# Optimization experiments

Hardware: AMD Instinct MI355X
Metric: run time of the kernel (lower is better)

The kernel has to match this reference:

```python
import jax, jax.numpy as jnp
import numpy as np

BATCH, IN_WIDTH, OUT_FEATURES, FAN_IN = 512, 4096, 4096, 128

def setup_inputs() -> dict:
    key = jax.random.key(0)
    k1, k2, k3, k4 = jax.random.split(key, 4)
    input = jax.random.normal(k1, (BATCH, IN_WIDTH), dtype=jnp.float32)
    weight = jax.random.normal(k2, (OUT_FEATURES, FAN_IN), dtype=jnp.float32)
    bias = jax.random.normal(k3, (OUT_FEATURES,), dtype=jnp.float32)
    indx_seqs = jax.random.randint(k4, (OUT_FEATURES, FAN_IN), 0, IN_WIDTH, dtype=jnp.int64)
    return {"input": input, "weight": weight, "bias": bias, "indx_seqs": indx_seqs}

def reference(input, weight, bias, indx_seqs):
    # gather: (B, out_features, fan_in)
    gathered = input[:, indx_seqs]
    # elementwise mul with weight (out_features, fan_in), reduce over fan_in
    return jnp.einsum('bof,of->bo', gathered, weight) + bias
```

## Files before the change

### kernel.cpp

```cpp
#include <hip/hip_runtime.h>
#include <hip/hip_bf16.h>

#define BATCH    512
#define IN_WIDTH 4096
#define OUT_F    4096
#define FAN_IN   128
#define BCHUNK   16
#define NBG      (BATCH / BCHUNK)
#define OBLK     512
#define NOG      (OUT_F / OBLK)

__global__ __launch_bounds__(256) void k_transpose_in(const float* __restrict__ in,
                                                      uint16_t* __restrict__ inTg) {
  __shared__ float tile[32][33];
  const int jt = blockIdx.x * 32;
  const int bt = blockIdx.y * 32;
  const int tx = threadIdx.x;
  const int ty = threadIdx.y;
#pragma unroll
  for (int r = 0; r < 32; r += 8) {
    tile[ty + r][tx] = in[(size_t)(bt + ty + r) * IN_WIDTH + (jt + tx)];
  }
  __syncthreads();
#pragma unroll
  for (int r = 0; r < 32; r += 8) {
    const int b = bt + tx;
    const int j = jt + ty + r;
    __hip_bfloat16 hv = __float2bfloat16(tile[tx][ty + r]);
    inTg[((size_t)(b >> 4) * IN_WIDTH + j) * BCHUNK + (b & 15)] =
        *reinterpret_cast<const uint16_t*>(&hv);
  }
}

__global__ __launch_bounds__(256) void k_pack(const int* __restrict__ idx,
                                              const float* __restrict__ weight,
                                              uint2* __restrict__ pk) {
  const int i = blockIdx.x * 256 + threadIdx.x;
  uint2 e;
  e.x = (uint32_t)idx[i];
  e.y = __float_as_uint(weight[i]);
  pk[i] = e;
}

__global__ __launch_bounds__(1024, 1) void k_gather_lds(const uint16_t* __restrict__ inTg,
                                                        const uint2* __restrict__ pk,
                                                        const float* __restrict__ bias,
                                                        float* __restrict__ outT) {
  extern __shared__ uint16_t inS[];
  const int og = blockIdx.x;
  const int bg = blockIdx.y;
  const int t  = threadIdx.x;

  {
    const uint4* __restrict__ src =
        reinterpret_cast<const uint4*>(inTg + (size_t)bg * IN_WIDTH * BCHUNK);
    uint4* dst = reinterpret_cast<uint4*>(inS);
#pragma unroll
    for (int i = 0; i < 8; ++i) {
      dst[i * 1024 + t] = src[i * 1024 + t];
    }
  }
  __syncthreads();

  const int wv = t >> 6;
  const int l  = t & 63;
  const int o  = og * OBLK + wv * 32 + (l >> 1);
  const int p  = l & 1;

  const uint4* __restrict__ pko = reinterpret_cast<const uint4*>(pk + (size_t)o * FAN_IN);
  const char* rowbase = reinterpret_cast<const char*>(inS) + p * 16;

  float a0 = 0.f, a1 = 0.f, a2 = 0.f, a3 = 0.f;
  float a4 = 0.f, a5 = 0.f, a6 = 0.f, a7 = 0.f;

#pragma unroll 2
  for (int f2 = 0; f2 < FAN_IN / 2; ++f2) {
    const uint4 q = pko[f2];
    {
      const uint4 v = *reinterpret_cast<const uint4*>(rowbase + q.x * 32);
      const float w = __uint_as_float(q.y);
      a0 = fmaf(__uint_as_float(v.x << 16),          w, a0);
      a1 = fmaf(__uint_as_float(v.x & 0xffff0000u),  w, a1);
      a2 = fmaf(__uint_as_float(v.y << 16),          w, a2);
      a3 = fmaf(__uint_as_float(v.y & 0xffff0000u),  w, a3);
      a4 = fmaf(__uint_as_float(v.z << 16),          w, a4);
      a5 = fmaf(__uint_as_float(v.z & 0xffff0000u),  w, a5);
      a6 = fmaf(__uint_as_float(v.w << 16),          w, a6);
      a7 = fmaf(__uint_as_float(v.w & 0xffff0000u),  w, a7);
    }
    {
      const uint4 v = *reinterpret_cast<const uint4*>(rowbase + q.z * 32);
      const float w = __uint_as_float(q.w);
      a0 = fmaf(__uint_as_float(v.x << 16),          w, a0);
      a1 = fmaf(__uint_as_float(v.x & 0xffff0000u),  w, a1);
      a2 = fmaf(__uint_as_float(v.y << 16),          w, a2);
      a3 = fmaf(__uint_as_float(v.y & 0xffff0000u),  w, a3);
      a4 = fmaf(__uint_as_float(v.z << 16),          w, a4);
      a5 = fmaf(__uint_as_float(v.z & 0xffff0000u),  w, a5);
      a6 = fmaf(__uint_as_float(v.w << 16),          w, a6);
      a7 = fmaf(__uint_as_float(v.w & 0xffff0000u),  w, a7);
    }
  }

  const float bz = bias[o];
  float4 r0 = make_float4(a0 + bz, a1 + bz, a2 + bz, a3 + bz);
  float4 r1 = make_float4(a4 + bz, a5 + bz, a6 + bz, a7 + bz);
  float4* dst = reinterpret_cast<float4*>(outT + (size_t)o * BATCH + bg * BCHUNK + p * 8);
  dst[0] = r0;
  dst[1] = r1;
}

__global__ __launch_bounds__(256) void k_transpose_out(const float* __restrict__ outT,
                                                       float* __restrict__ out) {
  __shared__ float tile[32][33];
  const int ot = blockIdx.x * 32;
  const int bt = blockIdx.y * 32;
  const int tx = threadIdx.x;
  const int ty = threadIdx.y;
#pragma unroll
  for (int r = 0; r < 32; r += 8) {
    tile[ty + r][tx] = outT[(size_t)(ot + ty + r) * BATCH + (bt + tx)];
  }
  __syncthreads();
#pragma unroll
  for (int r = 0; r < 32; r += 8) {
    out[(size_t)(bt + ty + r) * OUT_F + (ot + tx)] = tile[tx][ty + r];
  }
}

extern "C" void kernel_launch(void* const* d_in, const int* in_sizes, int n_in,
                              void* d_out, int out_size, void* d_ws, size_t ws_size,
                              hipStream_t stream) {
  const float* input  = (const float*)d_in[0];
  const float* weight = (const float*)d_in[1];
  const float* bias   = (const float*)d_in[2];
  const int*   idx    = (const int*)d_in[3];
  float* out = (float*)d_out;

  uint16_t* inTg = (uint16_t*)d_ws;
  float*    outT = (float*)((char*)d_ws + 4u * 1024 * 1024);
  uint2*    pk   = (uint2*)((char*)d_ws + 12u * 1024 * 1024);

  dim3 tblk(32, 8);
  k_transpose_in<<<dim3(IN_WIDTH / 32, BATCH / 32), tblk, 0, stream>>>(input, inTg);
  k_pack<<<dim3(OUT_F * FAN_IN / 256), dim3(256), 0, stream>>>(idx, weight, pk);
  k_gather_lds<<<dim3(NOG, NBG), dim3(1024), IN_WIDTH * BCHUNK * sizeof(uint16_t), stream>>>(
      inTg, pk, bias, outT);
  k_transpose_out<<<dim3(OUT_F / 32, BATCH / 32), tblk, 0, stream>>>(outT, out);
}
```

Before: 42.82 us.

## Fuse output transpose into gather kernel and pipeline LDS reads with packed FMA

Drops the separate output-transpose kernel and its intermediate buffer. The gather kernel now writes directly to the batch-major output with strided per-element stores. The inner loop is rewritten with inline ds_read_b128 and prefetching of the next index/weight chunk across an explicit waitcnt barrier. Accumulation uses 2-wide float vectors so the compiler can emit packed FMAs. This saves a launch and an output round trip through memory, but the direct stores write only one float per row per lane and are poorly coalesced.

```diff
diff --git a/kernel.cpp b/kernel.cpp
--- a/kernel.cpp
+++ b/kernel.cpp
@@ -9,6 +9,9 @@
 #define NBG      (BATCH / BCHUNK)
 #define OBLK     512
 #define NOG      (OUT_F / OBLK)
+
+typedef float    v2f __attribute__((ext_vector_type(2)));
+typedef uint32_t v4u __attribute__((ext_vector_type(4)));
 
 __global__ __launch_bounds__(256) void k_transpose_in(const float* __restrict__ in,
                                                       uint16_t* __restrict__ inTg) {
@@ -45,20 +48,18 @@
 __global__ __launch_bounds__(1024, 1) void k_gather_lds(const uint16_t* __restrict__ inTg,
                                                         const uint2* __restrict__ pk,
                                                         const float* __restrict__ bias,
-                                                        float* __restrict__ outT) {
-  extern __shared__ uint16_t inS[];
+                                                        float* __restrict__ out) {
+  extern __shared__ char lds[];
   const int og = blockIdx.x;
   const int bg = blockIdx.y;
   const int t  = threadIdx.x;
 
   {
-    const uint4* __restrict__ src =
-        reinterpret_cast<const uint4*>(inTg + (size_t)bg * IN_WIDTH * BCHUNK);
-    uint4* dst = reinterpret_cast<uint4*>(inS);
+    const v4u* __restrict__ src =
+        reinterpret_cast<const v4u*>(inTg + (size_t)bg * IN_WIDTH * BCHUNK);
+    v4u* dst = reinterpret_cast<v4u*>(lds);
 #pragma unroll
-    for (int i = 0; i < 8; ++i) {
-      dst[i * 1024 + t] = src[i * 1024 + t];
-    }
+    for (int i = 0; i < 8; ++i) dst[i * 1024 + t] = src[i * 1024 + t];
   }
   __syncthreads();
 
@@ -67,65 +68,71 @@
   const int o  = og * OBLK + wv * 32 + (l >> 1);
   const int p  = l & 1;
 
-  const uint4* __restrict__ pko = reinterpret_cast<const uint4*>(pk + (size_t)o * FAN_IN);
-  const char* rowbase = reinterpret_cast<const char*>(inS) + p * 16;
+  const uint32_t sb = (uint32_t)(size_t)lds + (uint32_t)(p * 16);
 
-  float a0 = 0.f, a1 = 0.f, a2 = 0.f, a3 = 0.f;
-  float a4 = 0.f, a5 = 0.f, a6 = 0.f, a7 = 0.f;
+  const v4u* __restrict__ pko =
+      reinterpret_cast<const v4u*>(pk + (size_t)o * FAN_IN);
 
-#pragma unroll 2
-  for (int f2 = 0; f2 < FAN_IN / 2; ++f2) {
-    const uint4 q = pko[f2];
-    {
-      const uint4 v = *reinterpret_cast<const uint4*>(rowbase + q.x * 32);
-      const float w = __uint_as_float(q.y);
-      a0 = fmaf(__uint_as_float(v.x << 16),          w, a0);
-      a1 = fmaf(__uint_as_float(v.x & 0xffff0000u),  w, a1);
-      a2 = fmaf(__uint_as_float(v.y << 16),          w, a2);
-      a3 = fmaf(__uint_as_float(v.y & 0xffff0000u),  w, a3);
-      a4 = fmaf(__uint_as_float(v.z << 16),          w, a4);
-      a5 = fmaf(__uint_as_float(v.z & 0xffff0000u),  w, a5);
-      a6 = fmaf(__uint_as_float(v.w << 16),          w, a6);
-      a7 = fmaf(__uint_as_float(v.w & 0xffff0000u),  w, a7);
-    }
-    {
-      const uint4 v = *reinterpret_cast<const uint4*>(rowbase + q.z * 32);
-      const float w = __uint_as_float(q.w);
-      a0 = fmaf(__uint_as_float(v.x << 16),          w, a0);
-      a1 = fmaf(__uint_as_float(v.x & 0xffff0000u),  w, a1);
-      a2 = fmaf(__uint_as_float(v.y << 16),          w, a2);
-      a3 = fmaf(__uint_as_float(v.y & 0xffff0000u),  w, a3);
-      a4 = fmaf(__uint_as_float(v.z << 16),          w, a4);
-      a5 = fmaf(__uint_as_float(v.z & 0xffff0000u),  w, a5);
-      a6 = fmaf(__uint_as_float(v.w << 16),          w, a6);
-      a7 = fmaf(__uint_as_float(v.w & 0xffff0000u),  w, a7);
-    }
+  v2f a0 = {0.f, 0.f}, a1 = {0.f, 0.f}, a2 = {0.f, 0.f}, a3 = {0.f, 0.f};
+
+#define DSREAD(dst, jj) \
+  asm volatile("ds_read_b128 %0, %1" : "=v"(dst) : "v"(sb + ((jj) << 5)))
+
+#define CONSUME(v, wbits)                                              \
+  do {                                                                 \
+    const float wf_ = __uint_as_float(wbits);                          \
+    v2f w2_; w2_[0] = wf_; w2_[1] = wf_;                               \
+    v2f x0_, x1_, x2_, x3_;                                            \
+    x0_[0] = __uint_as_float((v).x << 16);                             \
+    x0_[1] = __uint_as_float((v).x & 0xffff0000u);                     \
+    x1_[0] = __uint_as_float((v).y << 16);                             \
+    x1_[1] = __uint_as_float((v).y & 0xffff0000u);                     \
+    x2_[0] = __uint_as_float((v).z << 16);                             \
+    x2_[1] = __uint_as_float((v).z & 0xffff0000u);                     \
+    x3_[0] = __uint_as_float((v).w << 16);                             \
+    x3_[1] = __uint_as_float((v).w & 0xffff0000u);                     \
+    a0 += x0_ * w2_; a1 += x1_ * w2_; a2 += x2_ * w2_; a3 += x3_ * w2_;\
+  } while (0)
+
+#define HALF(qq0, qq1, qq2, qq3, nextchunk, more)                      \
+  do {                                                                 \
+    v4u v0, v1, v2, v3, v4, v5, v6, v7;                                \
+    DSREAD(v0, qq0.x); DSREAD(v1, qq0.z);                              \
+    DSREAD(v2, qq1.x); DSREAD(v3, qq1.z);                              \
+    DSREAD(v4, qq2.x); DSREAD(v5, qq2.z);                              \
+    DSREAD(v6, qq3.x); DSREAD(v7, qq3.z);                              \
+    const uint32_t w0 = qq0.y, w1 = qq0.w, w2 = qq1.y, w3 = qq1.w;     \
+    const uint32_t w4 = qq2.y, w5 = qq2.w, w6 = qq3.y, w7 = qq3.w;     \
+    if (more) {                                                        \
+      qq0 = pko[(nextchunk) * 4 + 0];                                  \
+      qq1 = pko[(nextchunk) * 4 + 1];                                  \
+      qq2 = pko[(nextchunk) * 4 + 2];                                  \
+      qq3 = pko[(nextchunk) * 4 + 3];                                  \
+    }                                                                  \
+    asm volatile("s_waitcnt lgkmcnt(0)" ::: "memory");                 \
+    __builtin_amdgcn_sched_barrier(0);                                 \
+    CONSUME(v0, w0); CONSUME(v1, w1); CONSUME(v2, w2); CONSUME(v3, w3);\
+    CONSUME(v4, w4); CONSUME(v5, w5); CONSUME(v6, w6); CONSUME(v7, w7);\
+  } while (0)
+
+  v4u qa0 = pko[0], qa1 = pko[1], qa2 = pko[2], qa3 = pko[3];
+  v4u qb0 = pko[4], qb1 = pko[5], qb2 = pko[6], qb3 = pko[7];
+
+#pragma unroll 1
+  for (int c = 0; c < 8; ++c) {
+    HALF(qa0, qa1, qa2, qa3, 2 * c + 2, (c < 7));
+    HALF(qb0, qb1, qb2, qb3, 2 * c + 3, (c < 7));
   }
 
   const float bz = bias[o];
-  float4 r0 = make_float4(a0 + bz, a1 + bz, a2 + bz, a3 + bz);
-  float4 r1 = make_float4(a4 + bz, a5 + bz, a6 + bz, a7 + bz);
-  float4* dst = reinterpret_cast<float4*>(outT + (size_t)o * BATCH + bg * BCHUNK + p * 8);
-  dst[0] = r0;
-  dst[1] = r1;
-}
+  const float r[8] = {a0[0], a0[1], a1[0], a1[1], a2[0], a2[1], a3[0], a3[1]};
+  const size_t obase = (size_t)(bg * BCHUNK + p * 8) * OUT_F + o;
+#pragma unroll
+  for (int i = 0; i < 8; ++i) out[obase + (size_t)i * OUT_F] = r[i] + bz;
 
-__global__ __launch_bounds__(256) void k_transpose_out(const float* __restrict__ outT,
-                                                       float* __restrict__ out) {
-  __shared__ float tile[32][33];
-  const int ot = blockIdx.x * 32;
-  const int bt = blockIdx.y * 32;
-  const int tx = threadIdx.x;
-  const int ty = threadIdx.y;
-#pragma unroll
-  for (int r = 0; r < 32; r += 8) {
-    tile[ty + r][tx] = outT[(size_t)(ot + ty + r) * BATCH + (bt + tx)];
-  }
-  __syncthreads();
-#pragma unroll
-  for (int r = 0; r < 32; r += 8) {
-    out[(size_t)(bt + ty + r) * OUT_F + (ot + tx)] = tile[tx][ty + r];
-  }
+#undef HALF
+#undef CONSUME
+#undef DSREAD
 }
 
 extern "C" void kernel_launch(void* const* d_in, const int* in_sizes, int n_in,
@@ -138,13 +145,11 @@
   float* out = (float*)d_out;
 
   uint16_t* inTg = (uint16_t*)d_ws;
-  float*    outT = (float*)((char*)d_ws + 4u * 1024 * 1024);
-  uint2*    pk   = (uint2*)((char*)d_ws + 12u * 1024 * 1024);
+  uint2*    pk   = (uint2*)((char*)d_ws + 4u * 1024 * 1024);
 
   dim3 tblk(32, 8);
   k_transpose_in<<<dim3(IN_WIDTH / 32, BATCH / 32), tblk, 0, stream>>>(input, inTg);
   k_pack<<<dim3(OUT_F * FAN_IN / 256), dim3(256), 0, stream>>>(idx, weight, pk);
-  k_gather_lds<<<dim3(NOG, NBG), dim3(1024), IN_WIDTH * BCHUNK * sizeof(uint16_t), stream>>>(
-      inTg, pk, bias, outT);
-  k_transpose_out<<<dim3(OUT_F / 32, BATCH / 32), tblk, 0, stream>>>(outT, out);
+  k_gather_lds<<<dim3(NOG, NBG), dim3(1024), IN_WIDTH * BCHUNK * 2, stream>>>(
+      inTg, pk, bias, out);
 }
```

New measurement: 67.38 us. 1.57x slower.
